# Performance work log

Hardware: AMD Instinct MI355X
Metric: run time of the kernel (lower is better)

## Reference

```python
import jax, jax.numpy as jnp
import numpy as np

N_EMBED = 512  # scaling uses n_embed**-0.5 (as in the original, not head_dim)

def setup_inputs() -> dict:
    key = jax.random.key(0)
    k1, k2, k3 = jax.random.split(key, 3)
    B, T, HD = 4, 4096, 64
    return {
        "k": jax.random.normal(k1, (B, T, HD), dtype=jnp.float32),
        "q": jax.random.normal(k2, (B, T, HD), dtype=jnp.float32),
        "v": jax.random.normal(k3, (B, T, HD), dtype=jnp.float32),
    }

def reference(k, q, v):
    # wei = q @ k^T * n_embed^-0.5  -> [B, T, T]
    scale = N_EMBED ** (-0.5)
    wei = jnp.einsum("bqd,bkd->bqk", q, k) * scale
    T = q.shape[1]
    causal = jnp.tril(jnp.ones((T, T), dtype=bool))  # [T, T]
    wei = jnp.where(causal, wei, -jnp.inf)
    wei = jax.nn.softmax(wei, axis=-1)
    # dropout p=0.0 (identity)
    out = jnp.einsum("bqk,bkd->bqd", wei, v)
    return out
```

## Files before the change

kernel.cpp:

```cpp
#include <hip/hip_runtime.h>
#include <hip/hip_bf16.h>
#include <math.h>


typedef __attribute__((ext_vector_type(8))) __bf16 bf16x8;
typedef __attribute__((ext_vector_type(8))) short  short8;
typedef __attribute__((ext_vector_type(4))) float  f32x4;

#define TT 4096
#define DD 64
#define NST 32
#define NCHUNK_PB 528
#define NSLOT (NCHUNK_PB * 4)

static constexpr float SCALE_L2E = 0.06375871665087779f;

__device__ __forceinline__ ushort f2bf(float x) {
    return __builtin_bit_cast(ushort, (__bf16)x);
}
__device__ __forceinline__ float bf2f(ushort u) {
    return __builtin_bit_cast(float, ((unsigned)u) << 16);
}

__global__ __launch_bounds__(256, 1)
void prep(const float* __restrict__ K, const float* __restrict__ V,
          ushort* __restrict__ Kbf, ushort* __restrict__ Vtbf) {
    const int bx = blockIdx.x;
    const int b = bx & 3, kt = bx >> 2;
    const size_t tbase = (size_t)bx * 4096;
    const size_t gbase = (size_t)b * TT * DD + (size_t)(kt << 6) * DD;
    const int tid = threadIdx.x;

    {
        const int row = tid >> 2, q4 = tid & 3;
        const float* src = K + gbase + row * 64 + q4 * 16;
        ushort* dst = Kbf + tbase + row * 64;
        #pragma unroll
        for (int h = 0; h < 2; ++h) {
            f32x4 x = *(const f32x4*)(src + h * 8);
            f32x4 y = *(const f32x4*)(src + h * 8 + 4);
            union { ushort u[8]; short8 s; } pk;
            #pragma unroll
            for (int j = 0; j < 4; ++j) {
                pk.u[j]     = f2bf(x[j]);
                pk.u[j + 4] = f2bf(y[j]);
            }
            const int ch = (q4 * 2 + h) ^ (row & 7);
            *(short8*)(dst + ch * 8) = pk.s;
        }
    }
    {
        const int kp = tid & 31, dg = tid >> 5;
        const float* v0 = V + gbase + dg * 8 + kp * 2 * 64;
        f32x4 a0 = *(const f32x4*)(v0);
        f32x4 a1 = *(const f32x4*)(v0 + 4);
        f32x4 b0 = *(const f32x4*)(v0 + 64);
        f32x4 b1 = *(const f32x4*)(v0 + 68);
        #pragma unroll
        for (int j = 0; j < 8; ++j) {
            float xa = (j < 4) ? a0[j & 3] : a1[j & 3];
            float xb = (j < 4) ? b0[j & 3] : b1[j & 3];
            unsigned pk2 = (unsigned)f2bf(xa) | ((unsigned)f2bf(xb) << 16);
            const int dim = dg * 8 + j;
            const int off = dim * 64 + (((kp >> 2) ^ j) << 3) + ((kp * 2) & 7);
            *(unsigned*)(Vtbf + tbase + off) = pk2;
        }
    }
}

__global__ __launch_bounds__(256, 4)
void attn_part(const ushort* __restrict__ Kbf, const float* __restrict__ Q,
               const ushort* __restrict__ Vtbf,
               ushort* __restrict__ Opart, float* __restrict__ Lpart) {
    const int bx = blockIdx.x;
    const int b  = bx & 3;
    const int chunkid = bx >> 2;
    int s = 0;
    while (chunkid >= ((s + 1) * (s + 2)) >> 1) ++s;
    const int chunk = chunkid - ((s * (s + 1)) >> 1);

    const int qs0 = s << 7;
    const int tid = threadIdx.x;
    const int w = tid >> 6, lane = tid & 63;
    const int g = lane >> 4, c = lane & 15;
    const int qw0 = qs0 + (w << 5);

    __shared__ ushort lKV[2][2][4096];
    __shared__ ushort lP [4][1024];

    const int kt0 = chunk * 2;
    const int seg0 = w * 1024;
    const int loff = lane * 8;

    {
        const size_t tb = (size_t)((kt0 << 2) | b) * 4096;
        #pragma unroll
        for (int p = 0; p < 2; ++p) {
            const int seg = seg0 + p * 512;
            __builtin_amdgcn_global_load_lds(
                (const __attribute__((address_space(1))) void*)(Kbf + tb + seg + loff),
                (__attribute__((address_space(3))) void*)&lKV[0][0][seg], 16, 0, 0);
            __builtin_amdgcn_global_load_lds(
                (const __attribute__((address_space(1))) void*)(Vtbf + tb + seg + loff),
                (__attribute__((address_space(3))) void*)&lKV[0][1][seg], 16, 0, 0);
        }
    }

    bf16x8 qf[2][2];
    #pragma unroll
    for (int m = 0; m < 2; ++m) {
        const float* qp = Q + (size_t)b * TT * DD
                        + (size_t)(qw0 + m * 16 + c) * DD + g * 8;
        #pragma unroll
        for (int ks = 0; ks < 2; ++ks) {
            f32x4 a = *(const f32x4*)(qp + ks * 32);
            f32x4 d = *(const f32x4*)(qp + ks * 32 + 4);
            bf16x8 t;
            #pragma unroll
            for (int j = 0; j < 4; ++j) {
                t[j]     = (__bf16)(a[j] * SCALE_L2E);
                t[j + 4] = (__bf16)(d[j] * SCALE_L2E);
            }
            qf[m][ks] = t;
        }
    }

    f32x4 acc[2][4];
    #pragma unroll
    for (int m = 0; m < 2; ++m)
        #pragma unroll
        for (int nt = 0; nt < 4; ++nt) acc[m][nt] = (f32x4){0.f, 0.f, 0.f, 0.f};
    float l_p[2][4] = {{0.f,0.f,0.f,0.f},{0.f,0.f,0.f,0.f}};

    #pragma unroll
    for (int st = 0; st < 2; ++st) {
        const int kt = kt0 + st;
        const int kb = kt << 6;

        __syncthreads();

        if (st == 0) {
            const size_t tb = (size_t)(((kt + 1) << 2) | b) * 4096;
            #pragma unroll
            for (int p = 0; p < 2; ++p) {
                const int seg = seg0 + p * 512;
                __builtin_amdgcn_global_load_lds(
                    (const __attribute__((address_space(1))) void*)(Kbf + tb + seg + loff),
                    (__attribute__((address_space(3))) void*)&lKV[1][0][seg], 16, 0, 0);
                __builtin_amdgcn_global_load_lds(
                    (const __attribute__((address_space(1))) void*)(Vtbf + tb + seg + loff),
                    (__attribute__((address_space(3))) void*)&lKV[1][1][seg], 16, 0, 0);
            }
        }

        if (kb > qw0 + 31) continue;
        const bool act0 = (kb <= qw0 + 15);

        const ushort* lK  = lKV[st][0];
        const ushort* lVt = lKV[st][1];

        f32x4 S[2][4];
        #pragma unroll
        for (int nt = 0; nt < 4; ++nt) {
            const int row = nt * 16 + c;
            bf16x8 kf0 = __builtin_bit_cast(bf16x8,
                *(const short8*)&lK[row * 64 + (((0 * 4 + g) ^ (c & 7)) << 3)]);
            bf16x8 kf1 = __builtin_bit_cast(bf16x8,
                *(const short8*)&lK[row * 64 + (((1 * 4 + g) ^ (c & 7)) << 3)]);
            #pragma unroll
            for (int m = 0; m < 2; ++m) {
                if (m == 0 && !act0) continue;
                f32x4 sm = (f32x4){0.f, 0.f, 0.f, 0.f};
                sm = __builtin_amdgcn_mfma_f32_16x16x32_bf16(qf[m][0], kf0, sm, 0, 0, 0);
                sm = __builtin_amdgcn_mfma_f32_16x16x32_bf16(qf[m][1], kf1, sm, 0, 0, 0);
                S[m][nt] = sm;
            }
        }

        bf16x8 pf[2][2];
        #pragma unroll
        for (int m = 0; m < 2; ++m) {
            if (m == 0 && !act0) continue;
            const int qm0 = qw0 + m * 16;
            if (kb + 63 > qm0) {
                #pragma unroll
                for (int nt = 0; nt < 4; ++nt)
                    #pragma unroll
                    for (int r = 0; r < 4; ++r)
                        if (kb + nt * 16 + c > qm0 + g * 4 + r) S[m][nt][r] = -INFINITY;
            }
            ushort* myP = lP[w];
            #pragma unroll
            for (int nt = 0; nt < 4; ++nt)
                #pragma unroll
                for (int r = 0; r < 4; ++r) {
                    const float P = exp2f(S[m][nt][r]);
                    l_p[m][r] += P;
                    const int row = g * 4 + r;
                    const int col = nt * 16 + c;
                    myP[row * 64 + (((col >> 3) ^ (row & 7)) << 3) + (col & 7)] =
                        f2bf(P);
                }
            #pragma unroll
            for (int ks = 0; ks < 2; ++ks)
                pf[m][ks] = __builtin_bit_cast(bf16x8,
                    *(const short8*)&myP[c * 64 + (((ks * 4 + g) ^ (c & 7)) << 3)]);
        }

        #pragma unroll
        for (int ks = 0; ks < 2; ++ks)
            #pragma unroll
            for (int nt = 0; nt < 4; ++nt) {
                bf16x8 vf = __builtin_bit_cast(bf16x8,
                    *(const short8*)&lVt[(nt * 16 + c) * 64 + (((ks * 4 + g) ^ (c & 7)) << 3)]);
                #pragma unroll
                for (int m = 0; m < 2; ++m) {
                    if (m == 0 && !act0) continue;
                    acc[m][nt] = __builtin_amdgcn_mfma_f32_16x16x32_bf16(
                        pf[m][ks], vf, acc[m][nt], 0, 0, 0);
                }
            }
    }

    const int slot = bx;
    #pragma unroll
    for (int m = 0; m < 2; ++m) {
        #pragma unroll
        for (int r = 0; r < 4; ++r) {
            float l = l_p[m][r];
            #pragma unroll
            for (int off = 8; off >= 1; off >>= 1)
                l += __shfl_xor(l, off);
            l_p[m][r] = l;
        }
        union { ushort u[16]; short8 s[2]; } pk;
        #pragma unroll
        for (int nt = 0; nt < 4; ++nt)
            #pragma unroll
            for (int r = 0; r < 4; ++r)
                pk.u[nt * 4 + r] = f2bf(acc[m][nt][r]);
        ushort* op = Opart + (size_t)slot * 8192 + (w * 2 + m) * 1024 + lane * 16;
        *(short8*)op       = pk.s[0];
        *(short8*)(op + 8) = pk.s[1];
        if (c == 0) {
            #pragma unroll
            for (int r = 0; r < 4; ++r)
                Lpart[(size_t)slot * 128 + w * 32 + m * 16 + g * 4 + r] = l_p[m][r];
        }
    }
}

__global__ __launch_bounds__(256, 1)
void attn_merge(const ushort* __restrict__ Opart, const float* __restrict__ Lpart,
                float* __restrict__ Out) {
    const int bx = blockIdx.x;
    const int b = bx & 3, s = (bx >> 2) & 31, w = bx >> 7;
    const int tid = threadIdx.x;
    const int m = tid >> 7, half = (tid >> 6) & 1, lane = tid & 63;
    const int g = lane >> 4, c = lane & 15;
    const int cbase = (s * (s + 1)) >> 1;
    const int nch = s + 1;

    float v[8];
    #pragma unroll
    for (int i = 0; i < 8; ++i) v[i] = 0.f;
    f32x4 lsum = (f32x4){0.f, 0.f, 0.f, 0.f};

    for (int ci = 0; ci < nch; ++ci) {
        const int slot = (cbase + ci) * 4 + b;
        const ushort* op = Opart + (size_t)slot * 8192
                         + (w * 2 + m) * 1024 + lane * 16 + half * 8;
        short8 sv = *(const short8*)op;
        #pragma unroll
        for (int i = 0; i < 8; ++i) v[i] += bf2f((ushort)sv[i]);
        f32x4 lv = *(const f32x4*)(Lpart + (size_t)slot * 128 + w * 32 + m * 16 + g * 4);
        #pragma unroll
        for (int r = 0; r < 4; ++r) lsum[r] += lv[r];
    }

    f32x4 inv;
    #pragma unroll
    for (int r = 0; r < 4; ++r) inv[r] = 1.0f / lsum[r];

    const int qbase = s * 128 + w * 32 + m * 16 + g * 4;
    float* dst = Out + (size_t)b * TT * DD;
    #pragma unroll
    for (int i = 0; i < 8; ++i) {
        const int nt = half * 2 + (i >> 2), r = i & 3;
        dst[(size_t)(qbase + r) * DD + nt * 16 + c] = v[i] * inv[r];
    }
}

__global__ __launch_bounds__(256, 1)
void attn_head(const float* __restrict__ K, const float* __restrict__ Q,
               const float* __restrict__ V, float* __restrict__ Out) {
    const int bx = blockIdx.x;
    const int b  = bx & 3;
    const int qt = bx >> 2;
    const int qbase = qt << 6;
    const int tid = threadIdx.x;
    const int w = tid >> 6, lane = tid & 63;
    const int g = lane >> 4, c = lane & 15;
    const int qr0 = qbase + (w << 4);

    __shared__ ushort lK [64 * 64];
    __shared__ ushort lVt[64 * 64];
    __shared__ ushort lP [4][16 * 64];

    const size_t bbase = (size_t)b * TT * DD;
    bf16x8 qf[2];
    {
        const float* qp = Q + bbase + (size_t)(qr0 + c) * DD + g * 8;
        #pragma unroll
        for (int ks = 0; ks < 2; ++ks) {
            f32x4 a = *(const f32x4*)(qp + ks * 32);
            f32x4 d = *(const f32x4*)(qp + ks * 32 + 4);
            bf16x8 t;
            #pragma unroll
            for (int j = 0; j < 4; ++j) {
                t[j]     = (__bf16)(a[j] * SCALE_L2E);
                t[j + 4] = (__bf16)(d[j] * SCALE_L2E);
            }
            qf[ks] = t;
        }
    }
    f32x4 acc[4];
    #pragma unroll
    for (int nt = 0; nt < 4; ++nt) acc[nt] = (f32x4){0.f, 0.f, 0.f, 0.f};
    float l_r[4] = {0.f, 0.f, 0.f, 0.f};
    const int e0  = w * 1024 + lane * 8;
    const int kch = ((lane & 7) ^ ((lane >> 3) & 7)) << 3;
    const int kp  = tid & 31, dg = tid >> 5;
    const int nkt = qt + 1;
    for (int kt = 0; kt < nkt; ++kt) {
        const int kb = kt << 6;
        __syncthreads();
        {
            const float* src = K + bbase + (size_t)kb * DD;
            #pragma unroll
            for (int p = 0; p < 2; ++p) {
                const int e = e0 + p * 512;
                f32x4 x = *(const f32x4*)(src + e);
                f32x4 y = *(const f32x4*)(src + e + 4);
                union { ushort u[8]; short8 s; } pk;
                #pragma unroll
                for (int j = 0; j < 4; ++j) {
                    pk.u[j]     = f2bf(x[j]);
                    pk.u[j + 4] = f2bf(y[j]);
                }
                *(short8*)&lK[(e >> 6) * 64 + kch] = pk.s;
            }
        }
        {
            const float* v0 = V + bbase + (size_t)kb * DD + dg * 8 + kp * 2 * 64;
            f32x4 a0 = *(const f32x4*)(v0);
            f32x4 a1 = *(const f32x4*)(v0 + 4);
            f32x4 b0 = *(const f32x4*)(v0 + 64);
            f32x4 b1 = *(const f32x4*)(v0 + 68);
            #pragma unroll
            for (int j = 0; j < 8; ++j) {
                float xa = (j < 4) ? a0[j & 3] : a1[j & 3];
                float xb = (j < 4) ? b0[j & 3] : b1[j & 3];
                unsigned pk2 = (unsigned)f2bf(xa) | ((unsigned)f2bf(xb) << 16);
                const int dim = dg * 8 + j;
                const int off = dim * 64 + (((kp >> 2) ^ j) << 3) + ((kp * 2) & 7);
                *(unsigned*)&lVt[off] = pk2;
            }
        }
        __syncthreads();
        if (kb <= qr0 + 15) {
            f32x4 S[4];
            #pragma unroll
            for (int nt = 0; nt < 4; ++nt) {
                const int row = nt * 16 + c;
                bf16x8 kf0 = __builtin_bit_cast(bf16x8,
                    *(const short8*)&lK[row * 64 + (((0 * 4 + g) ^ (c & 7)) << 3)]);
                bf16x8 kf1 = __builtin_bit_cast(bf16x8,
                    *(const short8*)&lK[row * 64 + (((1 * 4 + g) ^ (c & 7)) << 3)]);
                f32x4 sv = (f32x4){0.f, 0.f, 0.f, 0.f};
                sv = __builtin_amdgcn_mfma_f32_16x16x32_bf16(qf[0], kf0, sv, 0, 0, 0);
                sv = __builtin_amdgcn_mfma_f32_16x16x32_bf16(qf[1], kf1, sv, 0, 0, 0);
                S[nt] = sv;
            }
            if (kb + 63 > qr0) {
                #pragma unroll
                for (int nt = 0; nt < 4; ++nt)
                    #pragma unroll
                    for (int r = 0; r < 4; ++r)
                        if (kb + nt * 16 + c > qr0 + g * 4 + r) S[nt][r] = -INFINITY;
            }
            f32x4 P[4];
            #pragma unroll
            for (int nt = 0; nt < 4; ++nt)
                #pragma unroll
                for (int r = 0; r < 4; ++r)
                    P[nt][r] = exp2f(S[nt][r]);
            float ps[4];
            #pragma unroll
            for (int r = 0; r < 4; ++r)
                ps[r] = (P[0][r] + P[1][r]) + (P[2][r] + P[3][r]);
            #pragma unroll
            for (int off = 8; off >= 1; off >>= 1)
                #pragma unroll
                for (int r = 0; r < 4; ++r)
                    ps[r] += __shfl_xor(ps[r], off);
            #pragma unroll
            for (int r = 0; r < 4; ++r)
                l_r[r] += ps[r];
            ushort* myP = lP[w];
            #pragma unroll
            for (int nt = 0; nt < 4; ++nt)
                #pragma unroll
                for (int r = 0; r < 4; ++r) {
                    const int row = g * 4 + r;
                    const int col = nt * 16 + c;
                    myP[row * 64 + (((col >> 3) ^ (row & 7)) << 3) + (col & 7)] =
                        f2bf(P[nt][r]);
                }
            #pragma unroll
            for (int ks = 0; ks < 2; ++ks) {
                bf16x8 pf = __builtin_bit_cast(bf16x8,
                    *(const short8*)&myP[c * 64 + (((ks * 4 + g) ^ (c & 7)) << 3)]);
                #pragma unroll
                for (int nt = 0; nt < 4; ++nt) {
                    bf16x8 vf = __builtin_bit_cast(bf16x8,
                        *(const short8*)&lVt[(nt * 16 + c) * 64 + (((ks * 4 + g) ^ (c & 7)) << 3)]);
                    acc[nt] = __builtin_amdgcn_mfma_f32_16x16x32_bf16(pf, vf, acc[nt], 0, 0, 0);
                }
            }
        }
    }
    #pragma unroll
    for (int r = 0; r < 4; ++r) {
        const float inv = 1.0f / l_r[r];
        const size_t rowoff = bbase + (size_t)(qr0 + g * 4 + r) * DD;
        #pragma unroll
        for (int nt = 0; nt < 4; ++nt)
            Out[rowoff + nt * 16 + c] = acc[nt][r] * inv;
    }
}

extern "C" void kernel_launch(void* const* d_in, const int* in_sizes, int n_in,
                              void* d_out, int out_size, void* d_ws, size_t ws_size,
                              hipStream_t stream) {
    const float* k = (const float*)d_in[0];
    const float* q = (const float*)d_in[1];
    const float* v = (const float*)d_in[2];
    float* out = (float*)d_out;

    const size_t kv_elems = (size_t)4 * 64 * 4096;
    const size_t op_elems = (size_t)NSLOT * 8192;
    const size_t need = kv_elems * 2 * 2 + op_elems * 2 + (size_t)NSLOT * 128 * 4;
    if (ws_size >= need) {
        ushort* Kbf  = (ushort*)d_ws;
        ushort* Vtbf = Kbf + kv_elems;
        ushort* Opart = Vtbf + kv_elems;
        float* Lpart = (float*)(Opart + op_elems);
        hipLaunchKernelGGL(prep, dim3(256), dim3(256), 0, stream, k, v, Kbf, Vtbf);
        hipLaunchKernelGGL(attn_part, dim3(NSLOT), dim3(256), 0, stream,
                           Kbf, q, Vtbf, Opart, Lpart);
        hipLaunchKernelGGL(attn_merge, dim3(512), dim3(256), 0, stream,
                           Opart, Lpart, out);
    } else {
        hipLaunchKernelGGL(attn_head, dim3(256), dim3(256), 0, stream, k, q, v, out);
    }
}
```

Baseline: 106.3 us.

## Use larger KV chunks per block and fuse merge via last-block atomic counter

Each split-KV block now processes up to six key tiles instead of two, with a rolling double buffer, which cuts the number of partial outputs from 2112 to 748 slots. The separate merge kernel is removed. The last block to finish for each (query strip, batch) pair, found with an atomic counter that prep zeroes, performs the reduction and writes the output. This saves one kernel launch and a large amount of partial-result traffic, but it lengthens per-block work, adds tail imbalance and threadfence overhead, and lowers the occupancy hint from 4 to 3.

```diff
diff --git a/kernel.cpp b/kernel.cpp
--- a/kernel.cpp
+++ b/kernel.cpp
@@ -9,8 +9,8 @@
 
 #define TT 4096
 #define DD 64
-#define NST 32
-#define NCHUNK_PB 528
+#define CH 6
+#define NCHUNK_PB 187
 #define NSLOT (NCHUNK_PB * 4)
 
 static constexpr float SCALE_L2E = 0.06375871665087779f;
@@ -24,12 +24,15 @@
 
 __global__ __launch_bounds__(256, 1)
 void prep(const float* __restrict__ K, const float* __restrict__ V,
-          ushort* __restrict__ Kbf, ushort* __restrict__ Vtbf) {
+          ushort* __restrict__ Kbf, ushort* __restrict__ Vtbf,
+          int* __restrict__ Cnt) {
     const int bx = blockIdx.x;
     const int b = bx & 3, kt = bx >> 2;
     const size_t tbase = (size_t)bx * 4096;
     const size_t gbase = (size_t)b * TT * DD + (size_t)(kt << 6) * DD;
     const int tid = threadIdx.x;
+
+    if (bx == 0 && tid < 128) Cnt[tid] = 0;
 
     {
         const int row = tid >> 2, q4 = tid & 3;
@@ -68,27 +71,33 @@
     }
 }
 
-__global__ __launch_bounds__(256, 4)
+__global__ __launch_bounds__(256, 3)
 void attn_part(const ushort* __restrict__ Kbf, const float* __restrict__ Q,
                const ushort* __restrict__ Vtbf,
-               ushort* __restrict__ Opart, float* __restrict__ Lpart) {
+               ushort* __restrict__ Opart, float* __restrict__ Lpart,
+               int* __restrict__ Cnt, float* __restrict__ Out) {
     const int bx = blockIdx.x;
     const int b  = bx & 3;
     const int chunkid = bx >> 2;
-    int s = 0;
-    while (chunkid >= ((s + 1) * (s + 2)) >> 1) ++s;
-    const int chunk = chunkid - ((s * (s + 1)) >> 1);
-
-    const int qs0 = s << 7;
+    int s = 0, base = 0;
+    for (;;) {
+        const int nch = (s + 3) / 3;
+        if (chunkid < base + nch) break;
+        base += nch; ++s;
+    }
+    const int chunk = chunkid - base;
+
     const int tid = threadIdx.x;
     const int w = tid >> 6, lane = tid & 63;
     const int g = lane >> 4, c = lane & 15;
-    const int qw0 = qs0 + (w << 5);
+    const int qw0 = (s << 7) + (w << 5);
 
     __shared__ ushort lKV[2][2][4096];
     __shared__ ushort lP [4][1024];
-
-    const int kt0 = chunk * 2;
+    __shared__ int last_flag;
+
+    const int kt0 = chunk * CH;
+    const int nst = min(kt0 + CH, 2 * (s + 1)) - kt0;
     const int seg0 = w * 1024;
     const int loff = lane * 8;
 
@@ -132,32 +141,32 @@
         for (int nt = 0; nt < 4; ++nt) acc[m][nt] = (f32x4){0.f, 0.f, 0.f, 0.f};
     float l_p[2][4] = {{0.f,0.f,0.f,0.f},{0.f,0.f,0.f,0.f}};
 
-    #pragma unroll
-    for (int st = 0; st < 2; ++st) {
+    for (int st = 0; st < nst; ++st) {
         const int kt = kt0 + st;
         const int kb = kt << 6;
+        const int cur = st & 1;
 
         __syncthreads();
 
-        if (st == 0) {
+        if (st + 1 < nst) {
             const size_t tb = (size_t)(((kt + 1) << 2) | b) * 4096;
             #pragma unroll
             for (int p = 0; p < 2; ++p) {
                 const int seg = seg0 + p * 512;
                 __builtin_amdgcn_global_load_lds(
                     (const __attribute__((address_space(1))) void*)(Kbf + tb + seg + loff),
-                    (__attribute__((address_space(3))) void*)&lKV[1][0][seg], 16, 0, 0);
+                    (__attribute__((address_space(3))) void*)&lKV[cur ^ 1][0][seg], 16, 0, 0);
                 __builtin_amdgcn_global_load_lds(
                     (const __attribute__((address_space(1))) void*)(Vtbf + tb + seg + loff),
-                    (__attribute__((address_space(3))) void*)&lKV[1][1][seg], 16, 0, 0);
+                    (__attribute__((address_space(3))) void*)&lKV[cur ^ 1][1][seg], 16, 0, 0);
             }
         }
 
         if (kb > qw0 + 31) continue;
         const bool act0 = (kb <= qw0 + 15);
 
-        const ushort* lK  = lKV[st][0];
-        const ushort* lVt = lKV[st][1];
+        const ushort* lK  = lKV[cur][0];
+        const ushort* lVt = lKV[cur][1];
 
         f32x4 S[2][4];
         #pragma unroll
@@ -233,61 +242,64 @@
                 l += __shfl_xor(l, off);
             l_p[m][r] = l;
         }
-        union { ushort u[16]; short8 s[2]; } pk;
+        union { ushort u[16]; short8 s8[2]; } pk;
         #pragma unroll
         for (int nt = 0; nt < 4; ++nt)
             #pragma unroll
             for (int r = 0; r < 4; ++r)
                 pk.u[nt * 4 + r] = f2bf(acc[m][nt][r]);
         ushort* op = Opart + (size_t)slot * 8192 + (w * 2 + m) * 1024 + lane * 16;
-        *(short8*)op       = pk.s[0];
-        *(short8*)(op + 8) = pk.s[1];
+        *(short8*)op       = pk.s8[0];
+        *(short8*)(op + 8) = pk.s8[1];
         if (c == 0) {
             #pragma unroll
             for (int r = 0; r < 4; ++r)
-                Lpart[(size_t)slot * 128 + w * 32 + m * 16 + g * 4 + r] = l_p[m][r];
-        }
-    }
-}
-
-__global__ __launch_bounds__(256, 1)
-void attn_merge(const ushort* __restrict__ Opart, const float* __restrict__ Lpart,
-                float* __restrict__ Out) {
-    const int bx = blockIdx.x;
-    const int b = bx & 3, s = (bx >> 2) & 31, w = bx >> 7;
-    const int tid = threadIdx.x;
-    const int m = tid >> 7, half = (tid >> 6) & 1, lane = tid & 63;
-    const int g = lane >> 4, c = lane & 15;
-    const int cbase = (s * (s + 1)) >> 1;
-    const int nch = s + 1;
-
-    float v[8];
-    #pragma unroll
-    for (int i = 0; i < 8; ++i) v[i] = 0.f;
-    f32x4 lsum = (f32x4){0.f, 0.f, 0.f, 0.f};
-
-    for (int ci = 0; ci < nch; ++ci) {
-        const int slot = (cbase + ci) * 4 + b;
-        const ushort* op = Opart + (size_t)slot * 8192
-                         + (w * 2 + m) * 1024 + lane * 16 + half * 8;
-        short8 sv = *(const short8*)op;
-        #pragma unroll
-        for (int i = 0; i < 8; ++i) v[i] += bf2f((ushort)sv[i]);
-        f32x4 lv = *(const f32x4*)(Lpart + (size_t)slot * 128 + w * 32 + m * 16 + g * 4);
-        #pragma unroll
-        for (int r = 0; r < 4; ++r) lsum[r] += lv[r];
-    }
-
-    f32x4 inv;
-    #pragma unroll
-    for (int r = 0; r < 4; ++r) inv[r] = 1.0f / lsum[r];
-
-    const int qbase = s * 128 + w * 32 + m * 16 + g * 4;
-    float* dst = Out + (size_t)b * TT * DD;
-    #pragma unroll
-    for (int i = 0; i < 8; ++i) {
-        const int nt = half * 2 + (i >> 2), r = i & 3;
-        dst[(size_t)(qbase + r) * DD + nt * 16 + c] = v[i] * inv[r];
+                Lpart[(size_t)slot * 128 + (w * 2 + m) * 16 + g * 4 + r] = l_p[m][r];
+        }
+    }
+
+    __threadfence();
+    const int nch = (s + 3) / 3;
+    if (tid == 0) {
+        const int prev = atomicAdd(&Cnt[(s << 2) | b], 1);
+        last_flag = (prev == nch - 1);
+    }
+    __syncthreads();
+    if (!last_flag) return;
+    __threadfence();
+
+    #pragma unroll
+    for (int it = 0; it < 2; ++it) {
+        const int wm = (tid >> 6) * 2 + it;
+        const int ml = tid & 63, mg = ml >> 4, mc = ml & 15;
+        float v[16];
+        #pragma unroll
+        for (int i = 0; i < 16; ++i) v[i] = 0.f;
+        f32x4 lsum = (f32x4){0.f, 0.f, 0.f, 0.f};
+        for (int ci = 0; ci < nch; ++ci) {
+            const int sl = ((base + ci) << 2) | b;
+            const ushort* op = Opart + (size_t)sl * 8192 + wm * 1024 + ml * 16;
+            short8 s0 = *(const short8*)op;
+            short8 s1 = *(const short8*)(op + 8);
+            #pragma unroll
+            for (int i = 0; i < 8; ++i) {
+                v[i]     += bf2f((ushort)s0[i]);
+                v[i + 8] += bf2f((ushort)s1[i]);
+            }
+            f32x4 lv = *(const f32x4*)(Lpart + (size_t)sl * 128 + wm * 16 + mg * 4);
+            #pragma unroll
+            for (int r = 0; r < 4; ++r) lsum[r] += lv[r];
+        }
+        f32x4 inv;
+        #pragma unroll
+        for (int r = 0; r < 4; ++r) inv[r] = 1.0f / lsum[r];
+        float* dst = Out + (size_t)b * TT * DD;
+        #pragma unroll
+        for (int e = 0; e < 16; ++e) {
+            const int nt = e >> 2, r = e & 3;
+            dst[(size_t)((s << 7) + wm * 16 + mg * 4 + r) * DD + nt * 16 + mc] =
+                v[e] * inv[r];
+        }
     }
 }
 
@@ -450,17 +462,17 @@
 
     const size_t kv_elems = (size_t)4 * 64 * 4096;
     const size_t op_elems = (size_t)NSLOT * 8192;
-    const size_t need = kv_elems * 2 * 2 + op_elems * 2 + (size_t)NSLOT * 128 * 4;
+    const size_t l_elems  = (size_t)NSLOT * 128;
+    const size_t need = kv_elems * 2 * 2 + op_elems * 2 + l_elems * 4 + 128 * 4;
     if (ws_size >= need) {
-        ushort* Kbf  = (ushort*)d_ws;
-        ushort* Vtbf = Kbf + kv_elems;
+        ushort* Kbf   = (ushort*)d_ws;
+        ushort* Vtbf  = Kbf + kv_elems;
         ushort* Opart = Vtbf + kv_elems;
-        float* Lpart = (float*)(Opart + op_elems);
-        hipLaunchKernelGGL(prep, dim3(256), dim3(256), 0, stream, k, v, Kbf, Vtbf);
+        float*  Lpart = (float*)(Opart + op_elems);
+        int*    Cnt   = (int*)(Lpart + l_elems);
+        hipLaunchKernelGGL(prep, dim3(256), dim3(256), 0, stream, k, v, Kbf, Vtbf, Cnt);
         hipLaunchKernelGGL(attn_part, dim3(NSLOT), dim3(256), 0, stream,
-                           Kbf, q, Vtbf, Opart, Lpart);
-        hipLaunchKernelGGL(attn_merge, dim3(512), dim3(256), 0, stream,
-                           Opart, Lpart, out);
+                           Kbf, q, Vtbf, Opart, Lpart, Cnt, out);
     } else {
         hipLaunchKernelGGL(attn_head, dim3(256), dim3(256), 0, stream, k, q, v, out);
     }
```

Result: slower. 206.9 us (+94.6%).
